# Kernel optimization log

Hardware: AMD Instinct MI355X
Metric: run time of the kernel (lower is better)

The kernel has to match this reference:

```python
import math
import jax, jax.numpy as jnp
import numpy as np
from jax import lax

TAU = 1.0
LAMBDA_COUNT = 1.0
ALPHA = 0.85
GAMMA = 1.0
NUM_ITER = 40


def _minpool(x, wh, ww):
    # equals -max_pool2d(-x) in torch (padding acts as +inf for min)
    return lax.reduce_window(x, jnp.inf, lax.min, (1, 1, wh, ww), (1, 1, 1, 1),
                             [(0, 0), (0, 0), (wh // 2, wh // 2), (ww // 2, ww // 2)])


def _maxpool(x, wh, ww):
    return lax.reduce_window(x, -jnp.inf, lax.max, (1, 1, wh, ww), (1, 1, 1, 1),
                             [(0, 0), (0, 0), (wh // 2, wh // 2), (ww // 2, ww // 2)])


def soft_erode(img):
    return jnp.minimum(_minpool(img, 3, 1), _minpool(img, 1, 3))


def soft_dilate(img):
    return _maxpool(img, 3, 3)


def soft_open(img):
    return soft_dilate(soft_erode(img))


def soft_skel(img):
    skel = jax.nn.relu(img - soft_open(img))

    def step(carry, _):
        img, skel = carry
        img = soft_erode(img)
        delta = jax.nn.relu(img - soft_open(img))
        skel = skel + jax.nn.relu(delta - skel * delta)
        return (img, skel), None

    (_, skel), _ = lax.scan(step, (img, skel), None, length=NUM_ITER)
    return skel


def soft_endpoints(skel):
    kernel = jnp.ones((3, 3), dtype=skel.dtype).at[1, 1].set(10.0)[None, None]  # OIHW
    neighbor_sum = lax.conv_general_dilated(skel, kernel, (1, 1), [(1, 1), (1, 1)],
                                            dimension_numbers=('NCHW', 'OIHW', 'NCHW'))
    return jnp.exp(-GAMMA * (neighbor_sum - 11.0) ** 2) * skel


def weighted_coordinates(ep):
    # ep: [B,1,H,W] -> [B,2] (y,x) weighted mean coordinates
    B, _, H, W = ep.shape
    ys = jnp.arange(H, dtype=ep.dtype)
    xs = jnp.arange(W, dtype=ep.dtype)
    total = jnp.sum(ep, axis=(1, 2, 3)) + 1e-8  # [B]
    w = ep[:, 0] / total[:, None, None]  # [B,H,W]
    yc = jnp.sum(w * ys[:, None], axis=(1, 2))
    xc = jnp.sum(w * xs[None, :], axis=(1, 2))
    return jnp.stack([yc, xc], axis=1)


def soft_dice(y_true, y_pred):
    smooth = 1.0
    inter = jnp.sum(y_true * y_pred)
    coeff = (2.0 * inter + smooth) / (jnp.sum(y_true) + jnp.sum(y_pred) + smooth)
    return 1.0 - coeff


def setup_inputs() -> dict:
    key = jax.random.key(0)
    k1, k2 = jax.random.split(key)
    network_output = jax.random.normal(k1, (8, 2, 512, 512), dtype=jnp.float32)
    y_true = jax.random.randint(k2, (8, 1, 512, 512), 0, 2).astype(jnp.int32)
    return {"network_output": network_output, "y_true": y_true}


def reference(network_output, y_true):
    B, _, H, W = network_output.shape
    pred_prob_fg = jax.nn.softmax(network_output, axis=1)[:, 1:2]  # [B,1,H,W]
    y_true_f = y_true.astype(pred_prob_fg.dtype)

    skel_pred = soft_skel(pred_prob_fg)
    skel_true = soft_skel(y_true_f)

    ep_pred = soft_endpoints(skel_pred)
    ep_true = soft_endpoints(skel_true)

    # mismatch (distance) term
    pred_coords = weighted_coordinates(ep_pred)  # [B,2]
    true_coords = weighted_coordinates(ep_true)
    dist = jnp.sqrt(jnp.sum((pred_coords - true_coords) ** 2, axis=1))
    unnormalized_distance_loss = jnp.mean(dist)

    image_diagonal = math.sqrt(H ** 2 + W ** 2)
    distance_loss = unnormalized_distance_loss / (image_diagonal * TAU + 1e-8)

    n_pred = jnp.sum(ep_pred, axis=(1, 2, 3))
    n_true = jnp.sum(ep_true, axis=(1, 2, 3))
    count_penalty = jnp.mean(jnp.abs(n_pred - n_true) / (n_pred + n_true + 1e-8))

    final_endpoint_loss = distance_loss + LAMBDA_COUNT * count_penalty
    dice = soft_dice(y_true_f, pred_prob_fg)
    return ALPHA * dice + (1.0 - ALPHA) * final_endpoint_loss
```

## Files before the change

### kernel.cpp

```cpp
#include <hip/hip_runtime.h>
#include <math.h>

#define W 512
#define H 512
#define S (W * H)
#define B 8
#define NIMG 16
#define CORE 64
#define HALO 12
#define LDT 88
#define LROWS 90
#define NQ 22
#define FINF __builtin_huge_valf()

__device__ __forceinline__ float4 ld4s(const float* p) { return *(const float4*)p; }
__device__ __forceinline__ void st4s(float* p, float4 v) { *(float4*)p = v; }

__device__ __forceinline__ float blockReduce(float v, float* sw) {
    #pragma unroll
    for (int o = 32; o; o >>= 1) v += __shfl_down(v, o, 64);
    int lane = threadIdx.x & 63, wid = threadIdx.x >> 6;
    if (lane == 0) sw[wid] = v;
    __syncthreads();
    float r = (threadIdx.x < 4) ? sw[threadIdx.x] : 0.f;
    if (wid == 0) { r += __shfl_down(r, 2, 64); r += __shfl_down(r, 1, 64); }
    __syncthreads();
    return r;
}

__global__ __launch_bounds__(256) void phase1_kernel(
        const float* __restrict__ net, const int* __restrict__ yt,
        float* __restrict__ J0, double* __restrict__ pb,
        double* __restrict__ acc) {
    __shared__ float sw[4];
    const int tid = threadIdx.x;
    if (blockIdx.x == 0 && tid < 48) acc[tid] = 0.0;
    float inter = 0.f, sp = 0.f, sy = 0.f;
    for (int i = blockIdx.x * 256 + tid; i < B * S / 4; i += 1024 * 256) {
        int b = i >> 16;
        int s = (i & 65535) << 2;
        const float* nb = net + (size_t)b * 2 * S;
        float4 x0 = ld4s(nb + s);
        float4 x1 = ld4s(nb + S + s);
        int4 yv = *(const int4*)(yt + (size_t)b * S + s);
        float4 p, yf;
        p.x = 1.f / (1.f + expf(x0.x - x1.x));
        p.y = 1.f / (1.f + expf(x0.y - x1.y));
        p.z = 1.f / (1.f + expf(x0.z - x1.z));
        p.w = 1.f / (1.f + expf(x0.w - x1.w));
        yf.x = (float)yv.x; yf.y = (float)yv.y; yf.z = (float)yv.z; yf.w = (float)yv.w;
        st4s(J0 + (size_t)b * S + s, p);
        st4s(J0 + (size_t)(B + b) * S + s, yf);
        inter += p.x * yf.x + p.y * yf.y + p.z * yf.z + p.w * yf.w;
        sp += p.x + p.y + p.z + p.w;
        sy += yf.x + yf.y + yf.z + yf.w;
    }
    float v;
    v = blockReduce(inter, sw); if (tid == 0) pb[blockIdx.x * 3 + 0] = (double)v;
    v = blockReduce(sp, sw);    if (tid == 0) pb[blockIdx.x * 3 + 1] = (double)v;
    v = blockReduce(sy, sw);    if (tid == 0) pb[blockIdx.x * 3 + 2] = (double)v;
}

template <bool INIT>
__global__ __launch_bounds__(512, 6) void skel_fused_kernel(
        const float* __restrict__ Jin, float* __restrict__ Jout,
        float* __restrict__ skel, int r0) {
    __shared__ float Jl[LROWS * LDT];
    const int tid = threadIdx.x;
    const int lane = tid & 63;
    const int img = blockIdx.x >> 6;
    const int t64 = blockIdx.x & 63;
    const int ty = t64 >> 3, tx = t64 & 7;
    const int y0 = ty * CORE - HALO, x0 = tx * CORE - HALO;
    const float* Ji = Jin + (size_t)img * S;
    float* Jo = Jout + (size_t)img * S;
    float* Sk = skel + (size_t)img * S;
    const bool interior = (ty > 0) & (ty < 7) & (tx > 0) & (tx < 7);

    if (interior) {
        for (int i = tid; i < LDT * LDT / 4; i += 512) {
            int r = i / NQ, q = i - (i / NQ) * NQ;
            st4s(&Jl[r * LDT + (q << 2)],
                 ld4s(Ji + (y0 + r) * W + x0 + (q << 2)));
        }
    } else {
        for (int i = tid; i < LDT * LDT / 4; i += 512) {
            int r = i / NQ, q = i - (i / NQ) * NQ;
            int gy = y0 + r, gx = x0 + (q << 2);
            float4 v;
            if ((unsigned)gy < H && (unsigned)gx < W) v = ld4s(Ji + gy * W + gx);
            else v = make_float4(FINF, FINF, FINF, FINF);
            st4s(&Jl[r * LDT + (q << 2)], v);
        }
    }

    const int sq = tid & 15, ss = tid >> 4;
    const int tcol = HALO + (sq << 2);
    const int gxc = tx * CORE + (sq << 2);
    const int row0 = ss << 1;
    float4 sk2[2];
    #pragma unroll
    for (int j = 0; j < 2; ++j) {
        if (INIT) sk2[j] = make_float4(0.f, 0.f, 0.f, 0.f);
        else      sk2[j] = ld4s(Sk + (ty * CORE + row0 + j) * W + gxc);
    }
    __syncthreads();

    for (int rr = r0; rr < 6; ++rr) {
        const int rlo = 1 + 2 * rr, rhi = 86 - 2 * rr;
        const int qlo = rlo >> 2, qhi = rhi >> 2;
        const int nq = qhi - qlo + 1;
        const int nslab = (rhi - rlo + 1 + 3) >> 2;
        const int nit = nslab * nq;

        float4 Jst0 = ld4s(Jl + (row0 + 12) * LDT + tcol);
        float4 Jst1 = ld4s(Jl + (row0 + 13) * LDT + tcol);

        float4 Ereg[4];
        int rb = 0, cc = 0, qq = 0;
        const bool active = (tid < nit);
        if (active) {
            int sb = tid / nq;
            qq = qlo + (tid - sb * nq);
            rb = rlo + (sb << 2);
            cc = qq << 2;
            const float* bp = Jl + (rb - 1) * LDT + cc;
            float4 wA = ld4s(bp);
            float4 wB = ld4s(bp + LDT);
            const bool cOOB = (!interior) && ((unsigned)(x0 + cc) >= W);
            #pragma unroll
            for (int j = 0; j < 4; ++j) {
                float4 wC = ld4s(bp + (j + 2) * LDT);
                float lw = __shfl_up(wB.w, 1, 64);
                float rx = __shfl_down(wB.x, 1, 64);
                if (lane == 0 && qq != qlo)  lw = Jl[(rb + j) * LDT + cc - 1];
                if (lane == 63 && qq != qhi) rx = Jl[(rb + j) * LDT + cc + 4];
                if (qq == qlo) lw = FINF;
                if (qq == qhi) rx = FINF;
                float4 e;
                e.x = fminf(fminf(fminf(wA.x, wC.x), fminf(lw, wB.y)), wB.x);
                e.y = fminf(fminf(fminf(wA.y, wC.y), fminf(wB.x, wB.z)), wB.y);
                e.z = fminf(fminf(fminf(wA.z, wC.z), fminf(wB.y, wB.w)), wB.z);
                e.w = fminf(fminf(fminf(wA.w, wC.w), fminf(wB.z, rx)), wB.w);
                if (!interior) {
                    int gy = y0 + rb + j;
                    if (((unsigned)gy >= H) | cOOB)
                        e = make_float4(FINF, FINF, FINF, FINF);
                }
                Ereg[j] = e;
                wA = wB; wB = wC;
            }
        }
        __syncthreads();

        if (active) {
            #pragma unroll
            for (int j = 0; j < 4; ++j)
                if (rb + j <= rhi) st4s(&Jl[(rb + j) * LDT + cc], Ereg[j]);
        }
        __syncthreads();

        const bool last = (rr == 5);
        {
            const float* ebase = Jl + (row0 + 11) * LDT + tcol;
            float4 E[4];
            #pragma unroll
            for (int j = 0; j < 4; ++j) E[j] = ld4s(ebase + j * LDT);
            float lwv[4], rxv[4];
            #pragma unroll
            for (int j = 0; j < 4; ++j) {
                lwv[j] = __shfl_up(E[j].w, 1, 64);
                rxv[j] = __shfl_down(E[j].x, 1, 64);
                if (sq == 0)  lwv[j] = (tx == 0) ? -FINF : Jl[(row0 + 11 + j) * LDT + 11];
                if (sq == 15) rxv[j] = (tx == 7) ? -FINF : Jl[(row0 + 11 + j) * LDT + 76];
            }
            float4 hx[4];
            #pragma unroll
            for (int j = 0; j < 4; ++j) {
                hx[j].x = fmaxf(fmaxf(lwv[j], E[j].x), E[j].y);
                hx[j].y = fmaxf(fmaxf(E[j].x, E[j].y), E[j].z);
                hx[j].z = fmaxf(fmaxf(E[j].y, E[j].z), E[j].w);
                hx[j].w = fmaxf(fmaxf(E[j].z, E[j].w), rxv[j]);
            }
            #pragma unroll
            for (int j = 0; j < 2; ++j) {
                int gy = ty * CORE + row0 + j;
                float4 hm = hx[j], hp = hx[j + 2];
                if (!interior) {
                    if (gy == 0)     hm = make_float4(-FINF, -FINF, -FINF, -FINF);
                    if (gy == H - 1) hp = make_float4(-FINF, -FINF, -FINF, -FINF);
                }
                float4 dm;
                dm.x = fmaxf(fmaxf(hm.x, hx[j + 1].x), hp.x);
                dm.y = fmaxf(fmaxf(hm.y, hx[j + 1].y), hp.y);
                dm.z = fmaxf(fmaxf(hm.z, hx[j + 1].z), hp.z);
                dm.w = fmaxf(fmaxf(hm.w, hx[j + 1].w), hp.w);
                float4 Jv = (j == 0) ? Jst0 : Jst1;
                float d0 = fmaxf(Jv.x - dm.x, 0.f);
                float d1 = fmaxf(Jv.y - dm.y, 0.f);
                float d2 = fmaxf(Jv.z - dm.z, 0.f);
                float d3 = fmaxf(Jv.w - dm.w, 0.f);
                sk2[j].x += fmaxf(d0 - sk2[j].x * d0, 0.f);
                sk2[j].y += fmaxf(d1 - sk2[j].y * d1, 0.f);
                sk2[j].z += fmaxf(d2 - sk2[j].z * d2, 0.f);
                sk2[j].w += fmaxf(d3 - sk2[j].w * d3, 0.f);
                if (last) {
                    st4s(Jo + gy * W + gxc, E[j + 1]);
                    st4s(Sk + gy * W + gxc, sk2[j]);
                }
            }
        }
        if (!last) __syncthreads();
    }
}

__global__ __launch_bounds__(256) void endpoint_kernel(
        const float* __restrict__ skel, double* __restrict__ acc) {
    __shared__ float sR[10][520];
    __shared__ float sw[4];
    const int tid = threadIdx.x;
    const int img = blockIdx.x >> 6;
    const int rb = blockIdx.x & 63;
    const int yB = rb << 3;
    const float* Sk = skel + (size_t)img * S;
    for (int i = tid; i < 1280; i += 256) {
        int r = i >> 7, c4 = i & 127;
        int gy = yB - 1 + r;
        float4 v = make_float4(0.f, 0.f, 0.f, 0.f);
        if ((unsigned)gy < H) v = ld4s(Sk + gy * W + (c4 << 2));
        st4s(&sR[r][4 + (c4 << 2)], v);
    }
    if (tid < 10) { sR[tid][3] = 0.f; sR[tid][516] = 0.f; }
    __syncthreads();
    float t = 0.f, syA = 0.f, sxA = 0.f;
    #pragma unroll
    for (int k = 0; k < 4; ++k) {
        int qidx = k * 256 + tid;
        int rrow = qidx >> 7;
        int x = (qidx & 127) << 2;
        int r = 1 + rrow;
        float gy = (float)(yB + rrow);
        const float* Rm = &sR[r - 1][4 + x];
        const float* Rc = &sR[r][4 + x];
        const float* Rp = &sR[r + 1][4 + x];
        float4 bm = ld4s(Rm); float lm = ld4s(Rm - 4).w, rm = ld4s(Rm + 4).x;
        float4 bc = ld4s(Rc); float lc = ld4s(Rc - 4).w, rc = ld4s(Rc + 4).x;
        float4 bp = ld4s(Rp); float lp = ld4s(Rp - 4).w, rp = ld4s(Rp + 4).x;
        float hm0 = lm + bm.x + bm.y, hm1 = bm.x + bm.y + bm.z;
        float hm2 = bm.y + bm.z + bm.w, hm3 = bm.z + bm.w + rm;
        float hc0 = lc + bc.x + bc.y, hc1 = bc.x + bc.y + bc.z;
        float hc2 = bc.y + bc.z + bc.w, hc3 = bc.z + bc.w + rc;
        float hp0 = lp + bp.x + bp.y, hp1 = bp.x + bp.y + bp.z;
        float hp2 = bp.y + bp.z + bp.w, hp3 = bp.z + bp.w + rp;
        float ns0 = hm0 + hc0 + hp0 + 9.f * bc.x;
        float ns1 = hm1 + hc1 + hp1 + 9.f * bc.y;
        float ns2 = hm2 + hc2 + hp2 + 9.f * bc.z;
        float ns3 = hm3 + hc3 + hp3 + 9.f * bc.w;
        float e0 = ns0 - 11.f, e1 = ns1 - 11.f, e2 = ns2 - 11.f, e3 = ns3 - 11.f;
        float ep0 = expf(-e0 * e0) * bc.x;
        float ep1 = expf(-e1 * e1) * bc.y;
        float ep2 = expf(-e2 * e2) * bc.z;
        float ep3 = expf(-e3 * e3) * bc.w;
        float es = ep0 + ep1 + ep2 + ep3;
        t += es;
        syA += gy * es;
        sxA += ep0 * (float)(x + 0) + ep1 * (float)(x + 1)
             + ep2 * (float)(x + 2) + ep3 * (float)(x + 3);
    }
    float v;
    v = blockReduce(t, sw);   if (tid == 0) atomicAdd(&acc[img * 3 + 0], (double)v);
    v = blockReduce(syA, sw); if (tid == 0) atomicAdd(&acc[img * 3 + 1], (double)v);
    v = blockReduce(sxA, sw); if (tid == 0) atomicAdd(&acc[img * 3 + 2], (double)v);
}

__global__ __launch_bounds__(256) void final_kernel(
        const double* __restrict__ acc, const double* __restrict__ pb,
        float* __restrict__ out) {
    const int tid = threadIdx.x;
    double si = 0.0, sp = 0.0, sy = 0.0;
    for (int i = tid; i < 1024; i += 256) {
        si += pb[i * 3 + 0]; sp += pb[i * 3 + 1]; sy += pb[i * 3 + 2];
    }
    #pragma unroll
    for (int o = 32; o; o >>= 1) {
        si += __shfl_down(si, o, 64);
        sp += __shfl_down(sp, o, 64);
        sy += __shfl_down(sy, o, 64);
    }
    __shared__ double dsw[3][4];
    int lane = tid & 63, wid = tid >> 6;
    if (lane == 0) { dsw[0][wid] = si; dsw[1][wid] = sp; dsw[2][wid] = sy; }
    __syncthreads();
    if (tid == 0) {
        double inter = dsw[0][0] + dsw[0][1] + dsw[0][2] + dsw[0][3];
        double sump  = dsw[1][0] + dsw[1][1] + dsw[1][2] + dsw[1][3];
        double sumy  = dsw[2][0] + dsw[2][1] + dsw[2][2] + dsw[2][3];
        double dsum = 0.0, csum = 0.0;
        for (int b = 0; b < B; ++b) {
            double tp = acc[b * 3 + 0], typ = acc[b * 3 + 1], txp = acc[b * 3 + 2];
            double tt = acc[(B + b) * 3 + 0], tyt = acc[(B + b) * 3 + 1], txt = acc[(B + b) * 3 + 2];
            double ycp = typ / (tp + 1e-8), xcp = txp / (tp + 1e-8);
            double yct = tyt / (tt + 1e-8), xct = txt / (tt + 1e-8);
            double dy = ycp - yct, dx = xcp - xct;
            dsum += sqrt(dy * dy + dx * dx);
            csum += fabs(tp - tt) / (tp + tt + 1e-8);
        }
        double diag = sqrt((double)(H * H + W * W));
        double distance_loss = (dsum / B) / (diag + 1e-8);
        double count_penalty = csum / B;
        double dice = 1.0 - (2.0 * inter + 1.0) / (sumy + sump + 1.0);
        out[0] = (float)(0.85 * dice + 0.15 * (distance_loss + count_penalty));
    }
}

extern "C" void kernel_launch(void* const* d_in, const int* in_sizes, int n_in,
                              void* d_out, int out_size, void* d_ws, size_t ws_size,
                              hipStream_t stream) {
    const float* net = (const float*)d_in[0];
    const int*   yt  = (const int*)d_in[1];
    float* out = (float*)d_out;

    float* J0   = (float*)d_ws;
    float* J1   = J0 + (size_t)NIMG * S;
    float* skel = J1 + (size_t)NIMG * S;
    double* acc = (double*)(skel + (size_t)NIMG * S);
    double* pb  = acc + 48;

    phase1_kernel<<<1024, 256, 0, stream>>>(net, yt, J0, pb, acc);

    skel_fused_kernel<true><<<NIMG * 64, 512, 0, stream>>>(J0, J1, skel, 0);
    float* a = J1; float* b = J0;
    for (int p = 1; p < 7; ++p) {
        int r0 = (p == 6) ? 1 : 0;
        skel_fused_kernel<false><<<NIMG * 64, 512, 0, stream>>>(a, b, skel, r0);
        float* tmp = a; a = b; b = tmp;
    }

    endpoint_kernel<<<NIMG * 64, 256, 0, stream>>>(skel, acc);
    final_kernel<<<1, 256, 0, stream>>>(acc, pb, out);
}
```

Measured before the change: 344.7 us.

## Enlarge skeleton tile to 128x64 core to cut halo overhead

```diff
diff --git a/kernel.cpp b/kernel.cpp
--- a/kernel.cpp
+++ b/kernel.cpp
@@ -6,10 +6,11 @@
 #define S (W * H)
 #define B 8
 #define NIMG 16
-#define CORE 64
+#define CORE_Y 128
+#define CORE_X 64
 #define HALO 12
 #define LDT 88
-#define LROWS 90
+#define TROWS 154
 #define NQ 22
 #define FINF __builtin_huge_valf()
 
@@ -62,29 +63,29 @@
 }
 
 template <bool INIT>
-__global__ __launch_bounds__(512, 6) void skel_fused_kernel(
+__global__ __launch_bounds__(512, 4) void skel_fused_kernel(
         const float* __restrict__ Jin, float* __restrict__ Jout,
         float* __restrict__ skel, int r0) {
-    __shared__ float Jl[LROWS * LDT];
+    __shared__ float Jl[TROWS * LDT];
     const int tid = threadIdx.x;
     const int lane = tid & 63;
-    const int img = blockIdx.x >> 6;
-    const int t64 = blockIdx.x & 63;
-    const int ty = t64 >> 3, tx = t64 & 7;
-    const int y0 = ty * CORE - HALO, x0 = tx * CORE - HALO;
+    const int img = blockIdx.x >> 5;
+    const int t32 = blockIdx.x & 31;
+    const int ty = t32 >> 3, tx = t32 & 7;
+    const int y0 = ty * CORE_Y - HALO, x0 = tx * CORE_X - HALO;
     const float* Ji = Jin + (size_t)img * S;
     float* Jo = Jout + (size_t)img * S;
     float* Sk = skel + (size_t)img * S;
-    const bool interior = (ty > 0) & (ty < 7) & (tx > 0) & (tx < 7);
+    const bool interior = (ty > 0) & (ty < 3) & (tx > 0) & (tx < 7);
 
     if (interior) {
-        for (int i = tid; i < LDT * LDT / 4; i += 512) {
+        for (int i = tid; i < TROWS * NQ; i += 512) {
             int r = i / NQ, q = i - (i / NQ) * NQ;
             st4s(&Jl[r * LDT + (q << 2)],
                  ld4s(Ji + (y0 + r) * W + x0 + (q << 2)));
         }
     } else {
-        for (int i = tid; i < LDT * LDT / 4; i += 512) {
+        for (int i = tid; i < TROWS * NQ; i += 512) {
             int r = i / NQ, q = i - (i / NQ) * NQ;
             int gy = y0 + r, gx = x0 + (q << 2);
             float4 v;
@@ -96,95 +97,108 @@
 
     const int sq = tid & 15, ss = tid >> 4;
     const int tcol = HALO + (sq << 2);
-    const int gxc = tx * CORE + (sq << 2);
-    const int row0 = ss << 1;
-    float4 sk2[2];
-    #pragma unroll
-    for (int j = 0; j < 2; ++j) {
-        if (INIT) sk2[j] = make_float4(0.f, 0.f, 0.f, 0.f);
-        else      sk2[j] = ld4s(Sk + (ty * CORE + row0 + j) * W + gxc);
-    }
-    __syncthreads();
+    const int gxc = tx * CORE_X + (sq << 2);
+    const int trow = HALO + (ss << 2);
+    const int grow = ty * CORE_Y + (ss << 2);
+    float4 sk4[4];
+    #pragma unroll
+    for (int j = 0; j < 4; ++j) {
+        if (INIT) sk4[j] = make_float4(0.f, 0.f, 0.f, 0.f);
+        else      sk4[j] = ld4s(Sk + (grow + j) * W + gxc);
+    }
+    __syncthreads();
+
+    float4 Jc[4];
+    #pragma unroll
+    for (int j = 0; j < 4; ++j) Jc[j] = ld4s(Jl + (trow + j) * LDT + tcol);
 
     for (int rr = r0; rr < 6; ++rr) {
-        const int rlo = 1 + 2 * rr, rhi = 86 - 2 * rr;
-        const int qlo = rlo >> 2, qhi = rhi >> 2;
+        const int rlo = 1 + 2 * rr;
+        const int clo = 1 + 2 * rr, chi = 86 - 2 * rr;
+        const int qlo = clo >> 2, qhi = chi >> 2;
         const int nq = qhi - qlo + 1;
-        const int nslab = (rhi - rlo + 1 + 3) >> 2;
+        const int nslab = (152 - 4 * rr) >> 2;
         const int nit = nslab * nq;
 
-        float4 Jst0 = ld4s(Jl + (row0 + 12) * LDT + tcol);
-        float4 Jst1 = ld4s(Jl + (row0 + 13) * LDT + tcol);
-
-        float4 Ereg[4];
-        int rb = 0, cc = 0, qq = 0;
-        const bool active = (tid < nit);
-        if (active) {
-            int sb = tid / nq;
-            qq = qlo + (tid - sb * nq);
-            rb = rlo + (sb << 2);
-            cc = qq << 2;
-            const float* bp = Jl + (rb - 1) * LDT + cc;
-            float4 wA = ld4s(bp);
-            float4 wB = ld4s(bp + LDT);
-            const bool cOOB = (!interior) && ((unsigned)(x0 + cc) >= W);
-            #pragma unroll
-            for (int j = 0; j < 4; ++j) {
-                float4 wC = ld4s(bp + (j + 2) * LDT);
-                float lw = __shfl_up(wB.w, 1, 64);
-                float rx = __shfl_down(wB.x, 1, 64);
-                if (lane == 0 && qq != qlo)  lw = Jl[(rb + j) * LDT + cc - 1];
-                if (lane == 63 && qq != qhi) rx = Jl[(rb + j) * LDT + cc + 4];
-                if (qq == qlo) lw = FINF;
-                if (qq == qhi) rx = FINF;
-                float4 e;
-                e.x = fminf(fminf(fminf(wA.x, wC.x), fminf(lw, wB.y)), wB.x);
-                e.y = fminf(fminf(fminf(wA.y, wC.y), fminf(wB.x, wB.z)), wB.y);
-                e.z = fminf(fminf(fminf(wA.z, wC.z), fminf(wB.y, wB.w)), wB.z);
-                e.w = fminf(fminf(fminf(wA.w, wC.w), fminf(wB.z, rx)), wB.w);
-                if (!interior) {
-                    int gy = y0 + rb + j;
-                    if (((unsigned)gy >= H) | cOOB)
-                        e = make_float4(FINF, FINF, FINF, FINF);
+        float4 Er[2][4];
+        int rb_[2], cc_[2];
+        bool act_[2];
+        #pragma unroll
+        for (int s2 = 0; s2 < 2; ++s2) {
+            int it = tid + (s2 << 9);
+            const bool act = (it < nit);
+            act_[s2] = act;
+            if (act) {
+                int sb = it / nq;
+                int qq = qlo + (it - sb * nq);
+                int rb = rlo + (sb << 2);
+                int cc = qq << 2;
+                rb_[s2] = rb; cc_[s2] = cc;
+                const float* bp = Jl + (rb - 1) * LDT + cc;
+                float4 wA = ld4s(bp);
+                float4 wB = ld4s(bp + LDT);
+                const bool cOOB = (!interior) && ((unsigned)(x0 + cc) >= W);
+                #pragma unroll
+                for (int j = 0; j < 4; ++j) {
+                    float4 wC = ld4s(bp + (j + 2) * LDT);
+                    float lw = __shfl_up(wB.w, 1, 64);
+                    float rx = __shfl_down(wB.x, 1, 64);
+                    if (lane == 0 && qq != qlo)  lw = Jl[(rb + j) * LDT + cc - 1];
+                    if (lane == 63 && qq != qhi) rx = Jl[(rb + j) * LDT + cc + 4];
+                    if (qq == qlo) lw = FINF;
+                    if (qq == qhi) rx = FINF;
+                    float4 e;
+                    e.x = fminf(fminf(fminf(wA.x, wC.x), fminf(lw, wB.y)), wB.x);
+                    e.y = fminf(fminf(fminf(wA.y, wC.y), fminf(wB.x, wB.z)), wB.y);
+                    e.z = fminf(fminf(fminf(wA.z, wC.z), fminf(wB.y, wB.w)), wB.z);
+                    e.w = fminf(fminf(fminf(wA.w, wC.w), fminf(wB.z, rx)), wB.w);
+                    if (!interior) {
+                        int gy = y0 + rb + j;
+                        if (((unsigned)gy >= H) | cOOB)
+                            e = make_float4(FINF, FINF, FINF, FINF);
+                    }
+                    Er[s2][j] = e;
+                    wA = wB; wB = wC;
                 }
-                Ereg[j] = e;
-                wA = wB; wB = wC;
             }
         }
         __syncthreads();
 
-        if (active) {
-            #pragma unroll
-            for (int j = 0; j < 4; ++j)
-                if (rb + j <= rhi) st4s(&Jl[(rb + j) * LDT + cc], Ereg[j]);
+        #pragma unroll
+        for (int s2 = 0; s2 < 2; ++s2) {
+            if (act_[s2]) {
+                #pragma unroll
+                for (int j = 0; j < 4; ++j)
+                    st4s(&Jl[(rb_[s2] + j) * LDT + cc_[s2]], Er[s2][j]);
+            }
         }
         __syncthreads();
 
         const bool last = (rr == 5);
         {
-            const float* ebase = Jl + (row0 + 11) * LDT + tcol;
-            float4 E[4];
+            const float* ebase = Jl + (trow - 1) * LDT + tcol;
+            float4 E[6];
             #pragma unroll
-            for (int j = 0; j < 4; ++j) E[j] = ld4s(ebase + j * LDT);
-            float lwv[4], rxv[4];
+            for (int j = 0; j < 6; ++j) E[j] = ld4s(ebase + j * LDT);
+            float lwv[6], rxv[6];
             #pragma unroll
-            for (int j = 0; j < 4; ++j) {
+            for (int j = 0; j < 6; ++j) {
                 lwv[j] = __shfl_up(E[j].w, 1, 64);
                 rxv[j] = __shfl_down(E[j].x, 1, 64);
-                if (sq == 0)  lwv[j] = (tx == 0) ? -FINF : Jl[(row0 + 11 + j) * LDT + 11];
-                if (sq == 15) rxv[j] = (tx == 7) ? -FINF : Jl[(row0 + 11 + j) * LDT + 76];
-            }
-            float4 hx[4];
+                if (sq == 0)  lwv[j] = (tx == 0) ? -FINF : Jl[(trow - 1 + j) * LDT + 11];
+                if (sq == 15) rxv[j] = (tx == 7) ? -FINF : Jl[(trow - 1 + j) * LDT + 76];
+            }
+            float4 hx[6];
             #pragma unroll
-            for (int j = 0; j < 4; ++j) {
+            for (int j = 0; j < 6; ++j) {
                 hx[j].x = fmaxf(fmaxf(lwv[j], E[j].x), E[j].y);
                 hx[j].y = fmaxf(fmaxf(E[j].x, E[j].y), E[j].z);
                 hx[j].z = fmaxf(fmaxf(E[j].y, E[j].z), E[j].w);
                 hx[j].w = fmaxf(fmaxf(E[j].z, E[j].w), rxv[j]);
             }
             #pragma unroll
-            for (int j = 0; j < 2; ++j) {
-                int gy = ty * CORE + row0 + j;
+            for (int j = 0; j < 4; ++j) {
+                int gy = grow + j;
                 float4 hm = hx[j], hp = hx[j + 2];
                 if (!interior) {
                     if (gy == 0)     hm = make_float4(-FINF, -FINF, -FINF, -FINF);
@@ -195,18 +209,19 @@
                 dm.y = fmaxf(fmaxf(hm.y, hx[j + 1].y), hp.y);
                 dm.z = fmaxf(fmaxf(hm.z, hx[j + 1].z), hp.z);
                 dm.w = fmaxf(fmaxf(hm.w, hx[j + 1].w), hp.w);
-                float4 Jv = (j == 0) ? Jst0 : Jst1;
+                float4 Jv = Jc[j];
                 float d0 = fmaxf(Jv.x - dm.x, 0.f);
                 float d1 = fmaxf(Jv.y - dm.y, 0.f);
                 float d2 = fmaxf(Jv.z - dm.z, 0.f);
                 float d3 = fmaxf(Jv.w - dm.w, 0.f);
-                sk2[j].x += fmaxf(d0 - sk2[j].x * d0, 0.f);
-                sk2[j].y += fmaxf(d1 - sk2[j].y * d1, 0.f);
-                sk2[j].z += fmaxf(d2 - sk2[j].z * d2, 0.f);
-                sk2[j].w += fmaxf(d3 - sk2[j].w * d3, 0.f);
+                sk4[j].x += fmaxf(d0 - sk4[j].x * d0, 0.f);
+                sk4[j].y += fmaxf(d1 - sk4[j].y * d1, 0.f);
+                sk4[j].z += fmaxf(d2 - sk4[j].z * d2, 0.f);
+                sk4[j].w += fmaxf(d3 - sk4[j].w * d3, 0.f);
+                Jc[j] = E[j + 1];
                 if (last) {
                     st4s(Jo + gy * W + gxc, E[j + 1]);
-                    st4s(Sk + gy * W + gxc, sk2[j]);
+                    st4s(Sk + gy * W + gxc, sk4[j]);
                 }
             }
         }
@@ -328,11 +343,11 @@
 
     phase1_kernel<<<1024, 256, 0, stream>>>(net, yt, J0, pb, acc);
 
-    skel_fused_kernel<true><<<NIMG * 64, 512, 0, stream>>>(J0, J1, skel, 0);
+    skel_fused_kernel<true><<<NIMG * 32, 512, 0, stream>>>(J0, J1, skel, 0);
     float* a = J1; float* b = J0;
     for (int p = 1; p < 7; ++p) {
         int r0 = (p == 6) ? 1 : 0;
-        skel_fused_kernel<false><<<NIMG * 64, 512, 0, stream>>>(a, b, skel, r0);
+        skel_fused_kernel<false><<<NIMG * 32, 512, 0, stream>>>(a, b, skel, r0);
         float* tmp = a; a = b; b = tmp;
     }
 
```

New measurement: 347.5 us. About the same (+0.8%).
